# Performance work log

Measured on AMD Instinct MI355X. Metric: run time of the kernel, lower is better.

The kernel has to match this reference:

```python
import jax, jax.numpy as jnp
import numpy as np

P, N, C_IN = 30000, 64, 4     # pillars, max points per pillar, raw point features
OUT = 64                      # PFN output channels (must equal N for the original BN call)
C_AUG = C_IN + 5              # +3 cluster offsets, +2 center offsets
VX, VY = 0.2, 0.2
X_OFF = VX / 2 + 0.0          # pc_range x_min = 0
Y_OFF = VY / 2 + (-40.0)      # pc_range y_min = -40
EPS = 1e-3                    # BatchNorm eps from change_default_args


def setup_inputs() -> dict:
    key = jax.random.key(0)
    k1, k2, k3, k4, k5, k6 = jax.random.split(key, 6)
    features = jax.random.normal(k1, (P, N, C_IN), jnp.float32)
    num_points = jax.random.randint(k2, (P,), 1, N + 1, jnp.int32)  # >=1 to avoid div-by-zero
    coors = jax.random.randint(k3, (P, 4), 0, 352, jnp.int32)
    W = jax.random.normal(k4, (OUT, C_AUG), jnp.float32) * 0.1      # Linear(bias=False)
    gamma = 1.0 + 0.1 * jax.random.normal(k5, (OUT,), jnp.float32)  # BN weight
    beta = 0.1 * jax.random.normal(k6, (OUT,), jnp.float32)         # BN bias
    return {"features": features, "num_points": num_points, "coors": coors,
            "W": W, "gamma": gamma, "beta": beta}


def reference(features, num_points, coors, W, gamma, beta):
    dt = features.dtype
    npts = num_points.astype(dt)[:, None, None]                     # [P,1,1]
    xyz = features[:, :, :3]
    points_mean = xyz.sum(axis=1, keepdims=True) / npts             # [P,1,3]
    f_cluster = xyz - points_mean                                   # [P,N,3]
    cx = features[:, :, 0] - (coors[:, 3].astype(dt)[:, None] * VX + X_OFF)
    cy = features[:, :, 1] - (coors[:, 2].astype(dt)[:, None] * VY + Y_OFF)
    f_center = jnp.stack([cx, cy], axis=-1)                         # [P,N,2]
    feat = jnp.concatenate([features, f_cluster, f_center], axis=-1)  # [P,N,9]
    mask = (num_points[:, None] > jnp.arange(N, dtype=num_points.dtype))  # [P,N]
    feat = feat * mask[..., None].astype(dt)
    x = jnp.einsum('pnc,oc->pno', feat, W)                          # [P,N,OUT]
    # Faithful to the original: BatchNorm1d(OUT) applied WITHOUT permute, so the
    # channel axis is dim=1 (size N == OUT); training-mode batch stats over (P, last).
    mu = x.mean(axis=(0, 2), keepdims=True)                         # [1,N,1]
    var = x.var(axis=(0, 2), keepdims=True)                         # biased var, as BN
    x = (x - mu) * jax.lax.rsqrt(var + EPS) * gamma[None, :, None] + beta[None, :, None]
    x = jax.nn.relu(x)
    return x.max(axis=1)                                            # [P,OUT] (squeeze of keepdim max)
```

## Files before the change

kernel.cpp:

```cpp
#include <hip/hip_runtime.h>
#include <hip/hip_bf16.h>
#include <math.h>

typedef __attribute__((ext_vector_type(8))) __bf16 bf16x8;
typedef __attribute__((ext_vector_type(4))) float f32x4;

constexpr float VX_ = 0.2f;
constexpr float VY_ = 0.2f;
constexpr float X_OFF_ = 0.1f;
constexpr float Y_OFF_ = -39.9f;
constexpr float EPS_ = 1e-3f;

#define S1 512

__device__ __forceinline__ float wave_sum(float v) {
#pragma unroll
  for (int off = 32; off; off >>= 1) v += __shfl_xor(v, off);
  return v;
}

__device__ __forceinline__ ushort bf16bits(float x) {
  __hip_bfloat16 h = __float2bfloat16(x);
  return __builtin_bit_cast(ushort, h);
}

__device__ __forceinline__ uint32_t cvtpk(float lo, float hi) {
  uint32_t r;
  asm("v_cvt_pk_bf16_f32 %0, %1, %2" : "=v"(r) : "v"(lo), "v"(hi));
  return r;
}

__global__ __launch_bounds__(256) void k1_moments(
    const float* __restrict__ feats, const int* __restrict__ npts_arr,
    const int* __restrict__ coors, const float* __restrict__ W,
    float* __restrict__ partials, float* __restrict__ aux,
    uint32_t* __restrict__ Bpack, int P) {
  __shared__ float W_lds[576];
  __shared__ float gws[54];
  __shared__ float2 red[4][64];
  const int t = threadIdx.x, lane = t & 63, wv = t >> 6;

  for (int i = t; i < 576; i += 256) W_lds[i] = W[i];
  __syncthreads();
  if (t < 180) {
    const int pr = t >> 2, k = t & 3;
    int c = 0, rem = pr;
    while (rem >= 9 - c) {
      rem -= 9 - c;
      ++c;
    }
    const int c2 = c + rem;
    float s = 0.f;
    for (int o = k * 16; o < k * 16 + 16; ++o)
      s += W_lds[o * 9 + c] * W_lds[o * 9 + c2];
    s += __shfl_xor(s, 1);
    s += __shfl_xor(s, 2);
    if (k == 0) gws[pr] = (c == c2) ? s : 2.f * s;
  } else if (t < 216) {
    const int tt = t - 180, c = tt >> 2, k = tt & 3;
    float s = 0.f;
    for (int o = k * 16; o < k * 16 + 16; ++o) s += W_lds[o * 9 + c];
    s += __shfl_xor(s, 1);
    s += __shfl_xor(s, 2);
    if (k == 0) gws[45 + c] = s;
  }
  __syncthreads();
  float g[45], wsv[9];
#pragma unroll
  for (int i = 0; i < 45; ++i) g[i] = gws[i];
#pragma unroll
  for (int i = 0; i < 9; ++i) wsv[i] = gws[45 + i];

  if (blockIdx.x == 0) {
    const int nt = t >> 6, bl = t & 63;
    const int l16 = bl & 15, g16 = bl >> 4;
    const int col = nt * 16 + l16;
    ushort h[8];
#pragma unroll
    for (int j = 0; j < 8; ++j) {
      const int kk = 8 * g16 + j;
      h[j] = (kk < 9) ? bf16bits(W_lds[col * 9 + kk])
                      : ((kk == 9) ? bf16bits(1.0f) : (ushort)0);
    }
    uint4 q;
    q.x = (uint)h[0] | ((uint)h[1] << 16);
    q.y = (uint)h[2] | ((uint)h[3] << 16);
    q.z = (uint)h[4] | ((uint)h[5] << 16);
    q.w = (uint)h[6] | ((uint)h[7] << 16);
    *reinterpret_cast<uint4*>(Bpack + (size_t)t * 4) = q;
  }

  float s1 = 0.f, s2 = 0.f;
  const int nw = S1 * 4;
  int p = blockIdx.x * 4 + wv;
  if (p < P) {
    float4 f =
        *reinterpret_cast<const float4*>(feats + (size_t)p * 256 + lane * 4);
    int np = npts_arr[p];
    int cx = coors[p * 4 + 3], cy = coors[p * 4 + 2];
    while (true) {
      const int p2 = p + nw;
      const bool has2 = p2 < P;
      float4 f2 = make_float4(0.f, 0.f, 0.f, 0.f);
      int np2 = 1, cx2 = 0, cy2 = 0;
      if (has2) {
        f2 = *reinterpret_cast<const float4*>(feats + (size_t)p2 * 256 +
                                              lane * 4);
        np2 = npts_arr[p2];
        cx2 = coors[p2 * 4 + 3];
        cy2 = coors[p2 * 4 + 2];
      }
      const float ox = (float)cx * VX_ + X_OFF_;
      const float oy = (float)cy * VY_ + Y_OFF_;
      const float inv = 1.f / (float)np;
      const float m0 = wave_sum(f.x) * inv;
      const float m1 = wave_sum(f.y) * inv;
      const float m2 = wave_sum(f.z) * inv;
      if (lane == 0) {
        *reinterpret_cast<float4*>(aux + (size_t)p * 8) =
            make_float4(m0, m1, m2, ox);
        *reinterpret_cast<float4*>(aux + (size_t)p * 8 + 4) =
            make_float4(oy, __int_as_float(np), 0.f, 0.f);
      }
      const bool valid = lane < np;
      float ft[9] = {f.x,      f.y,      f.z,      f.w,      f.x - m0,
                     f.y - m1, f.z - m2, f.x - ox, f.y - oy};
#pragma unroll
      for (int c = 0; c < 9; ++c) ft[c] = valid ? ft[c] : 0.f;
      int idx = 0;
      float t1 = 0.f, t2 = 0.f;
#pragma unroll
      for (int c = 0; c < 9; ++c) {
        float u = 0.f;
#pragma unroll
        for (int c2 = c; c2 < 9; ++c2) u = fmaf(g[idx++], ft[c2], u);
        t2 = fmaf(ft[c], u, t2);
        t1 = fmaf(ft[c], wsv[c], t1);
      }
      s1 += t1;
      s2 += t2;
      if (!has2) break;
      p = p2;
      f = f2;
      np = np2;
      cx = cx2;
      cy = cy2;
    }
  }
  red[wv][lane] = make_float2(s1, s2);
  __syncthreads();
  if (t < 64) {
    const float v = red[0][t].x + red[1][t].x + red[2][t].x + red[3][t].x;
    partials[((size_t)t * 2 + 0) * S1 + blockIdx.x] = v;
  } else if (t < 128) {
    const int n = t - 64;
    const float v = red[0][n].y + red[1][n].y + red[2][n].y + red[3][n].y;
    partials[((size_t)n * 2 + 1) * S1 + blockIdx.x] = v;
  }
}

__global__ __launch_bounds__(256) void k2_stats(
    const float* __restrict__ partials, const float* __restrict__ gamma,
    const float* __restrict__ beta, float* __restrict__ ab, int P) {
  const int n = blockIdx.x, t = threadIdx.x;
  __shared__ float r1[4], r2[4];
  const float* p1 = partials + ((size_t)n * 2 + 0) * S1;
  const float* p2 = partials + ((size_t)n * 2 + 1) * S1;
  float a1 = 0.f, a2 = 0.f;
  for (int b = t; b < S1; b += 256) {
    a1 += p1[b];
    a2 += p2[b];
  }
  a1 = wave_sum(a1);
  a2 = wave_sum(a2);
  const int wv = t >> 6;
  if ((t & 63) == 0) {
    r1[wv] = a1;
    r2[wv] = a2;
  }
  __syncthreads();
  if (t == 0) {
    const float v2 = r1[0] + r1[1] + r1[2] + r1[3];
    const float v1 = r2[0] + r2[1] + r2[2] + r2[3];
    const float invPN = 1.f / ((float)P * 64.f);
    const float mu = v2 * invPN;
    const float var = v1 * invPN - mu * mu;
    const float a = gamma[n] * rsqrtf(var + EPS_);
    const float b = beta[n] - mu * a;
    ab[n] = a;
    ab[64 + n] = b;
  }
}

__global__ __launch_bounds__(256) void k4_mfma(
    const float* __restrict__ feats, const float* __restrict__ aux,
    const uint32_t* __restrict__ Bpack, const float* __restrict__ ab,
    float* __restrict__ out, int P) {
  __shared__ uint32_t A_lds[4][64][20];
  const int t = threadIdx.x, lane = t & 63, wv = t >> 6;
  const int g16 = lane >> 4, l16 = lane & 15;

  uint4 bq[4];
#pragma unroll
  for (int nt = 0; nt < 4; ++nt)
    bq[nt] =
        *reinterpret_cast<const uint4*>(Bpack + ((size_t)nt * 64 + lane) * 4);
  const float a_l = ab[lane];
  const float b_l = ab[64 + lane];

  A_lds[wv][lane][5] = 0u;
  A_lds[wv][lane][6] = 0u;
  A_lds[wv][lane][7] = 0u;
  *reinterpret_cast<uint4*>(&A_lds[wv][lane][8]) = make_uint4(0u, 0u, 0u, 0u);
  *reinterpret_cast<uint4*>(&A_lds[wv][lane][12]) = make_uint4(0u, 0u, 0u, 0u);

  const int p = blockIdx.x * 4 + wv;
  if (p >= P) return;
  const float4 f =
      *reinterpret_cast<const float4*>(feats + (size_t)p * 256 + lane * 4);
  const float4 a0 = *reinterpret_cast<const float4*>(aux + (size_t)p * 8);
  const float4 a1 = *reinterpret_cast<const float4*>(aux + (size_t)p * 8 + 4);

  const float m0 = a0.x, m1 = a0.y, m2 = a0.z, ox = a0.w, oy = a1.x;
  const int np = __float_as_int(a1.y);
  const bool valid = lane < np;
  const float v0 = valid ? a_l * f.x : 0.f;
  const float v1 = valid ? a_l * f.y : 0.f;
  const float v2 = valid ? a_l * f.z : 0.f;
  const float v3 = valid ? a_l * f.w : 0.f;
  const float v4 = valid ? a_l * (f.x - m0) : 0.f;
  const float v5 = valid ? a_l * (f.y - m1) : 0.f;
  const float v6 = valid ? a_l * (f.z - m2) : 0.f;
  const float v7 = valid ? a_l * (f.x - ox) : 0.f;
  const float v8 = valid ? a_l * (f.y - oy) : 0.f;
  union {
    uint32_t u[6];
    uint4 q;
  } pk;
  pk.u[0] = cvtpk(v0, v1);
  pk.u[1] = cvtpk(v2, v3);
  pk.u[2] = cvtpk(v4, v5);
  pk.u[3] = cvtpk(v6, v7);
  pk.u[4] = cvtpk(v8, b_l);
  *reinterpret_cast<uint4*>(&A_lds[wv][lane][0]) = pk.q;
  A_lds[wv][lane][4] = pk.u[4];

  bf16x8 afr[4];
#pragma unroll
  for (int mt = 0; mt < 4; ++mt) {
    afr[mt] =
        *reinterpret_cast<const bf16x8*>(&A_lds[wv][mt * 16 + l16][g16 * 4]);
  }
  const f32x4 accz = {0.f, 0.f, 0.f, 0.f};
  float mx[4] = {0.f, 0.f, 0.f, 0.f};
#pragma unroll
  for (int mt = 0; mt < 4; ++mt) {
    const bf16x8 a = afr[mt];
#pragma unroll
    for (int nt = 0; nt < 4; ++nt) {
      f32x4 acc4 = __builtin_amdgcn_mfma_f32_16x16x32_bf16(
          a, __builtin_bit_cast(bf16x8, bq[nt]), accz, 0, 0, 0);
#pragma unroll
      for (int r = 0; r < 4; ++r) mx[nt] = fmaxf(mx[nt], acc4[r]);
    }
  }
#pragma unroll
  for (int nt = 0; nt < 4; ++nt) {
    mx[nt] = fmaxf(mx[nt], __shfl_xor(mx[nt], 16));
    mx[nt] = fmaxf(mx[nt], __shfl_xor(mx[nt], 32));
  }
  const float outv =
      (g16 == 0) ? mx[0] : (g16 == 1) ? mx[1] : (g16 == 2) ? mx[2] : mx[3];
  out[(size_t)p * 64 + lane] = outv;
}

extern "C" void kernel_launch(void* const* d_in, const int* in_sizes, int n_in,
                              void* d_out, int out_size, void* d_ws,
                              size_t ws_size, hipStream_t stream) {
  const float* feats = (const float*)d_in[0];
  const int* npts = (const int*)d_in[1];
  const int* coors = (const int*)d_in[2];
  const float* W = (const float*)d_in[3];
  const float* gamma = (const float*)d_in[4];
  const float* beta = (const float*)d_in[5];
  float* out = (float*)d_out;
  float* ws = (float*)d_ws;

  const int P = in_sizes[1];

  float* ab = ws;
  uint32_t* Bpack = (uint32_t*)(ws + 128);
  float* partials = ws + 128 + 1024;
  float* aux = partials + 64 * 2 * S1;

  k1_moments<<<S1, 256, 0, stream>>>(feats, npts, coors, W, partials, aux,
                                     Bpack, P);
  k2_stats<<<64, 256, 0, stream>>>(partials, gamma, beta, ab, P);
  const int g1 = (P + 3) / 4;
  k4_mfma<<<g1, 256, 0, stream>>>(feats, aux, Bpack, ab, out, P);
}
```

Baseline: 39.75 us.

## Raise moment-kernel grid size adaptively and use DPP wave reductions

The stats kernel's block count becomes a runtime parameter of up to 2048 blocks (was 512), shrunk only if the workspace is too small. The aux and partials buffers are reordered so partials can grow. Wave sums in the moment pass move from shuffle-xor to DPP row operations plus a readlane. The intent is more parallelism in the memory-bound first pass and cheaper cross-lane reductions, at the cost of more partials for the second kernel to reduce.

```diff
diff --git a/kernel.cpp b/kernel.cpp
--- a/kernel.cpp
+++ b/kernel.cpp
@@ -11,12 +11,28 @@
 constexpr float Y_OFF_ = -39.9f;
 constexpr float EPS_ = 1e-3f;
 
-#define S1 512
-
 __device__ __forceinline__ float wave_sum(float v) {
 #pragma unroll
   for (int off = 32; off; off >>= 1) v += __shfl_xor(v, off);
   return v;
+}
+
+template <int CTRL, int RMASK>
+__device__ __forceinline__ float dpp_add(float x) {
+  const int xi = __builtin_bit_cast(int, x);
+  const int yi = __builtin_amdgcn_update_dpp(0, xi, CTRL, RMASK, 0xf, false);
+  return x + __builtin_bit_cast(float, yi);
+}
+
+__device__ __forceinline__ float wave_sum_dpp(float v) {
+  v = dpp_add<0x111, 0xf>(v);
+  v = dpp_add<0x112, 0xf>(v);
+  v = dpp_add<0x114, 0xf>(v);
+  v = dpp_add<0x118, 0xf>(v);
+  v = dpp_add<0x142, 0xa>(v);
+  v = dpp_add<0x143, 0xc>(v);
+  return __builtin_bit_cast(
+      float, __builtin_amdgcn_readlane(__builtin_bit_cast(int, v), 63));
 }
 
 __device__ __forceinline__ ushort bf16bits(float x) {
@@ -34,7 +50,7 @@
     const float* __restrict__ feats, const int* __restrict__ npts_arr,
     const int* __restrict__ coors, const float* __restrict__ W,
     float* __restrict__ partials, float* __restrict__ aux,
-    uint32_t* __restrict__ Bpack, int P) {
+    uint32_t* __restrict__ Bpack, int S, int P) {
   __shared__ float W_lds[576];
   __shared__ float gws[54];
   __shared__ float2 red[4][64];
@@ -91,7 +107,7 @@
   }
 
   float s1 = 0.f, s2 = 0.f;
-  const int nw = S1 * 4;
+  const int nw = S * 4;
   int p = blockIdx.x * 4 + wv;
   if (p < P) {
     float4 f =
@@ -113,9 +129,9 @@
       const float ox = (float)cx * VX_ + X_OFF_;
       const float oy = (float)cy * VY_ + Y_OFF_;
       const float inv = 1.f / (float)np;
-      const float m0 = wave_sum(f.x) * inv;
-      const float m1 = wave_sum(f.y) * inv;
-      const float m2 = wave_sum(f.z) * inv;
+      const float m0 = wave_sum_dpp(f.x) * inv;
+      const float m1 = wave_sum_dpp(f.y) * inv;
+      const float m2 = wave_sum_dpp(f.z) * inv;
       if (lane == 0) {
         *reinterpret_cast<float4*>(aux + (size_t)p * 8) =
             make_float4(m0, m1, m2, ox);
@@ -151,23 +167,23 @@
   __syncthreads();
   if (t < 64) {
     const float v = red[0][t].x + red[1][t].x + red[2][t].x + red[3][t].x;
-    partials[((size_t)t * 2 + 0) * S1 + blockIdx.x] = v;
+    partials[((size_t)t * 2 + 0) * S + blockIdx.x] = v;
   } else if (t < 128) {
     const int n = t - 64;
     const float v = red[0][n].y + red[1][n].y + red[2][n].y + red[3][n].y;
-    partials[((size_t)n * 2 + 1) * S1 + blockIdx.x] = v;
+    partials[((size_t)n * 2 + 1) * S + blockIdx.x] = v;
   }
 }
 
 __global__ __launch_bounds__(256) void k2_stats(
     const float* __restrict__ partials, const float* __restrict__ gamma,
-    const float* __restrict__ beta, float* __restrict__ ab, int P) {
+    const float* __restrict__ beta, float* __restrict__ ab, int S, int P) {
   const int n = blockIdx.x, t = threadIdx.x;
   __shared__ float r1[4], r2[4];
-  const float* p1 = partials + ((size_t)n * 2 + 0) * S1;
-  const float* p2 = partials + ((size_t)n * 2 + 1) * S1;
+  const float* p1 = partials + ((size_t)n * 2 + 0) * S;
+  const float* p2 = partials + ((size_t)n * 2 + 1) * S;
   float a1 = 0.f, a2 = 0.f;
-  for (int b = t; b < S1; b += 256) {
+  for (int b = t; b < S; b += 256) {
     a1 += p1[b];
     a2 += p2[b];
   }
@@ -290,12 +306,18 @@
 
   float* ab = ws;
   uint32_t* Bpack = (uint32_t*)(ws + 128);
-  float* partials = ws + 128 + 1024;
-  float* aux = partials + 64 * 2 * S1;
-
-  k1_moments<<<S1, 256, 0, stream>>>(feats, npts, coors, W, partials, aux,
-                                     Bpack, P);
-  k2_stats<<<64, 256, 0, stream>>>(partials, gamma, beta, ab, P);
+  float* aux = ws + 128 + 1024;
+  float* partials = aux + 8 * (size_t)P;
+
+  int S = 2048;
+  while (S > 1 &&
+         (size_t)(128 + 1024 + 8 * (size_t)P + 64 * 2 * (size_t)S) * 4 >
+             ws_size)
+    S >>= 1;
+
+  k1_moments<<<S, 256, 0, stream>>>(feats, npts, coors, W, partials, aux,
+                                    Bpack, S, P);
+  k2_stats<<<64, 256, 0, stream>>>(partials, gamma, beta, ab, S, P);
   const int g1 = (P + 3) / 4;
   k4_mfma<<<g1, 256, 0, stream>>>(feats, aux, Bpack, ab, out, P);
 }
```

Measured after the change: 40.62 us. 2.2% more time.

## Fuse BN stats reduction into moments kernel via atomics and last-block finalize

Applied to the files above, without the earlier changes.

Removes the separate k2_stats launch. Each block atomically adds its per-channel sums into one of NREP replicated accumulators, and the last block to arrive, detected through an atomic counter, finalizes mean, variance and the affine coefficients. This trades one kernel launch and its partials traffic for a memset, atomic contention and a serialized tail in the final block. Float atomics also make the summation order nondeterministic.

```diff
diff --git a/kernel.cpp b/kernel.cpp
--- a/kernel.cpp
+++ b/kernel.cpp
@@ -12,6 +12,7 @@
 constexpr float EPS_ = 1e-3f;
 
 #define S1 512
+#define NREP 8
 
 __device__ __forceinline__ float wave_sum(float v) {
 #pragma unroll
@@ -33,11 +34,14 @@
 __global__ __launch_bounds__(256) void k1_moments(
     const float* __restrict__ feats, const int* __restrict__ npts_arr,
     const int* __restrict__ coors, const float* __restrict__ W,
-    float* __restrict__ partials, float* __restrict__ aux,
+    const float* __restrict__ gamma, const float* __restrict__ beta,
+    float* __restrict__ accrep, unsigned int* __restrict__ counter,
+    float* __restrict__ ab, float* __restrict__ aux,
     uint32_t* __restrict__ Bpack, int P) {
   __shared__ float W_lds[576];
   __shared__ float gws[54];
   __shared__ float2 red[4][64];
+  __shared__ int lastflag;
   const int t = threadIdx.x, lane = t & 63, wv = t >> 6;
 
   for (int i = t; i < 576; i += 256) W_lds[i] = W[i];
@@ -149,46 +153,42 @@
   }
   red[wv][lane] = make_float2(s1, s2);
   __syncthreads();
-  if (t < 64) {
-    const float v = red[0][t].x + red[1][t].x + red[2][t].x + red[3][t].x;
-    partials[((size_t)t * 2 + 0) * S1 + blockIdx.x] = v;
-  } else if (t < 128) {
-    const int n = t - 64;
-    const float v = red[0][n].y + red[1][n].y + red[2][n].y + red[3][n].y;
-    partials[((size_t)n * 2 + 1) * S1 + blockIdx.x] = v;
-  }
-}
-
-__global__ __launch_bounds__(256) void k2_stats(
-    const float* __restrict__ partials, const float* __restrict__ gamma,
-    const float* __restrict__ beta, float* __restrict__ ab, int P) {
-  const int n = blockIdx.x, t = threadIdx.x;
-  __shared__ float r1[4], r2[4];
-  const float* p1 = partials + ((size_t)n * 2 + 0) * S1;
-  const float* p2 = partials + ((size_t)n * 2 + 1) * S1;
-  float a1 = 0.f, a2 = 0.f;
-  for (int b = t; b < S1; b += 256) {
-    a1 += p1[b];
-    a2 += p2[b];
-  }
-  a1 = wave_sum(a1);
-  a2 = wave_sum(a2);
-  const int wv = t >> 6;
-  if ((t & 63) == 0) {
-    r1[wv] = a1;
-    r2[wv] = a2;
+  if (t < 128) {
+    const int n = t & 63, j = t >> 6;
+    const float v = (j == 0)
+                        ? (red[0][n].x + red[1][n].x + red[2][n].x + red[3][n].x)
+                        : (red[0][n].y + red[1][n].y + red[2][n].y + red[3][n].y);
+    atomicAdd(&accrep[(blockIdx.x & (NREP - 1)) * 128 + t], v);
   }
   __syncthreads();
   if (t == 0) {
-    const float v2 = r1[0] + r1[1] + r1[2] + r1[3];
-    const float v1 = r2[0] + r2[1] + r2[2] + r2[3];
-    const float invPN = 1.f / ((float)P * 64.f);
-    const float mu = v2 * invPN;
-    const float var = v1 * invPN - mu * mu;
-    const float a = gamma[n] * rsqrtf(var + EPS_);
-    const float b = beta[n] - mu * a;
-    ab[n] = a;
-    ab[64 + n] = b;
+    __threadfence();
+    const unsigned int old = __hip_atomic_fetch_add(
+        counter, 1u, __ATOMIC_ACQ_REL, __HIP_MEMORY_SCOPE_AGENT);
+    lastflag = (old == (unsigned int)(S1 - 1)) ? 1 : 0;
+  }
+  __syncthreads();
+  if (lastflag) {
+    __threadfence();
+    float* tf = reinterpret_cast<float*>(red);
+    if (t < 128) {
+      float s = 0.f;
+#pragma unroll
+      for (int r = 0; r < NREP; ++r)
+        s += __hip_atomic_load(&accrep[r * 128 + t], __ATOMIC_RELAXED,
+                               __HIP_MEMORY_SCOPE_AGENT);
+      tf[t] = s;
+    }
+    __syncthreads();
+    if (t < 64) {
+      const float sx = tf[t], sxx = tf[64 + t];
+      const float invPN = 1.f / ((float)P * 64.f);
+      const float mu = sx * invPN;
+      const float var = sxx * invPN - mu * mu;
+      const float a = gamma[t] * rsqrtf(var + EPS_);
+      ab[t] = a;
+      ab[64 + t] = beta[t] - mu * a;
+    }
   }
 }
 
@@ -288,14 +288,15 @@
 
   const int P = in_sizes[1];
 
-  float* ab = ws;
-  uint32_t* Bpack = (uint32_t*)(ws + 128);
-  float* partials = ws + 128 + 1024;
-  float* aux = partials + 64 * 2 * S1;
-
-  k1_moments<<<S1, 256, 0, stream>>>(feats, npts, coors, W, partials, aux,
-                                     Bpack, P);
-  k2_stats<<<64, 256, 0, stream>>>(partials, gamma, beta, ab, P);
+  float* accrep = ws;
+  unsigned int* counter = (unsigned int*)(ws + NREP * 128);
+  float* ab = ws + NREP * 128 + 64;
+  uint32_t* Bpack = (uint32_t*)(ws + NREP * 128 + 64 + 128);
+  float* aux = ws + NREP * 128 + 64 + 128 + 1024;
+
+  hipMemsetAsync(accrep, 0, (NREP * 128 + 1) * sizeof(float), stream);
+  k1_moments<<<S1, 256, 0, stream>>>(feats, npts, coors, W, gamma, beta,
+                                     accrep, counter, ab, aux, Bpack, P);
   const int g1 = (P + 3) / 4;
   k4_mfma<<<g1, 256, 0, stream>>>(feats, aux, Bpack, ab, out, P);
 }
```

Result: slower. 61.42 us (+54.5%).
